# Optimization experiments

Measured on AMD Instinct MI355X. Metric: run time of the kernel, lower is better.

## Reference

```python
import jax, jax.numpy as jnp
import numpy as np

NW, NT, ND = 100000, 10000, 50000
D = 128
E = {"ww": 200000, "wt": 100000, "wd": 150000, "td": 100000, "tt": 50000}


def setup_inputs() -> dict:
    key = jax.random.key(0)
    ks = iter(jax.random.split(key, 40))
    inp = {
        "h_word": jax.random.normal(next(ks), (NW, D), dtype=jnp.float32),
        "h_topic": jax.random.normal(next(ks), (NT, D), dtype=jnp.float32),
        "h_doc": jax.random.normal(next(ks), (ND, D), dtype=jnp.float32),
    }
    for et in ["ww", "wt", "wd", "td", "tt"]:
        inp[f"W_{et}"] = jax.random.normal(next(ks), (D, D), dtype=jnp.float32) * 0.05
        inp[f"b_{et}"] = jax.random.normal(next(ks), (D,), dtype=jnp.float32) * 0.05
    sizes = {"ww": (NW, NW), "wt": (NW, NT), "wd": (NW, ND), "td": (NT, ND), "tt": (NT, NT)}
    for et, (ns, nd) in sizes.items():
        inp[f"src_{et}"] = jax.random.randint(next(ks), (E[et],), 0, ns, dtype=jnp.int32)
        inp[f"dst_{et}"] = jax.random.randint(next(ks), (E[et],), 0, nd, dtype=jnp.int32)
        inp[f"ew_{et}"] = jax.random.uniform(next(ks), (E[et],), dtype=jnp.float32)
    return inp


def _linear(x, W, b):
    # torch nn.Linear: y = x @ W.T + b, W is [out, in]
    return x @ W.T + b


def _mean_agg(h_src, src, dst, ew, n_dst):
    # message m_e = h_src[src_e] * ew_e (u_mul_e), then per-dst mean (fn.mean)
    m = h_src[src] * ew[:, None]                               # [E, D]
    s = jax.ops.segment_sum(m, dst, num_segments=n_dst)        # [n_dst, D]
    cnt = jax.ops.segment_sum(jnp.ones_like(ew), dst, num_segments=n_dst)
    return s / jnp.maximum(cnt, 1.0)[:, None]


def reference(h_word, h_topic, h_doc,
              W_ww, b_ww, W_wt, b_wt, W_wd, b_wd, W_td, b_td, W_tt, b_tt,
              src_ww, dst_ww, ew_ww, src_wt, dst_wt, ew_wt,
              src_wd, dst_wd, ew_wd, src_td, dst_td, ew_td,
              src_tt, dst_tt, ew_tt):
    # DGL loop overwrites src node 'h' in-place -> linears COMPOSE per src type,
    # and messages (resolved at multi_update_all) use the final composed 'h'.
    hw = _linear(_linear(_linear(h_word, W_ww, b_ww), W_wt, b_wt), W_wd, b_wd)
    ht = _linear(_linear(h_topic, W_td, b_td), W_tt, b_tt)
    nw, nt, nd = h_word.shape[0], h_topic.shape[0], h_doc.shape[0]
    # cross-relation 'sum' of per-relation means
    out_word = _mean_agg(hw, src_ww, dst_ww, ew_ww, nw)
    out_topic = _mean_agg(hw, src_wt, dst_wt, ew_wt, nt) + _mean_agg(ht, src_tt, dst_tt, ew_tt, nt)
    out_doc = _mean_agg(hw, src_wd, dst_wd, ew_wd, nd) + _mean_agg(ht, src_td, dst_td, ew_td, nd)
    # relu + dropout (eval mode -> identity); concatenate node types for a single output
    return jnp.concatenate([
        jax.nn.relu(out_word), jax.nn.relu(out_topic), jax.nn.relu(out_doc)
    ], axis=0)
```

## Files before the change

kernel.cpp:

```cpp
#include <hip/hip_runtime.h>
#include <hip/hip_bf16.h>

#define DIM 128
#define NWORD 100000
#define NTOPIC 10000
#define NDOC 50000
#define NOUT (NWORD + NTOPIC + NDOC)

#define E_WW 200000
#define E_WT 100000
#define E_WD 150000
#define E_TD 100000
#define E_TT 50000
#define E_TOT 600000

#define B_WW 0
#define B_WT 100000
#define B_TT 110000
#define B_WD 120000
#define B_TD 170000
#define NSLOT 220000
#define NBLK_SCAN 215

typedef __attribute__((ext_vector_type(8))) short bf16x8;
typedef __attribute__((ext_vector_type(8))) unsigned short u16x8;
typedef __attribute__((ext_vector_type(4))) float f32x4;

__device__ __forceinline__ unsigned short f2bf(float f) {
    __hip_bfloat16 h = __float2bfloat16(f);
    return __builtin_bit_cast(unsigned short, h);
}
__device__ __forceinline__ float b2f(unsigned short u) {
    return __builtin_bit_cast(float, (unsigned)u << 16);
}

__global__ void compose1(const float* __restrict__ W_ww, const float* __restrict__ b_ww,
                         const float* __restrict__ W_wt, const float* __restrict__ b_wt,
                         const float* __restrict__ W_wd, const float* __restrict__ b_wd,
                         const float* __restrict__ W_td, const float* __restrict__ b_td,
                         const float* __restrict__ W_tt, const float* __restrict__ b_tt,
                         float* __restrict__ A, unsigned short* __restrict__ Wbf_t,
                         float* __restrict__ tmpb, float* __restrict__ c_t)
{
    int b = blockIdx.x, j = threadIdx.x;
    if (b < 128) {
        float s = 0.f;
        for (int m = 0; m < 128; ++m) s = fmaf(W_wd[b * 128 + m], W_wt[m * 128 + j], s);
        A[b * 128 + j] = s;
    } else if (b < 256) {
        int k = b - 128;
        float s = 0.f;
        for (int m = 0; m < 128; ++m) s = fmaf(W_tt[j * 128 + m], W_td[m * 128 + k], s);
        Wbf_t[j * 128 + k] = f2bf(s);
    } else if (b == 256) {
        float s = b_wt[j];
        for (int m = 0; m < 128; ++m) s = fmaf(W_wt[j * 128 + m], b_ww[m], s);
        tmpb[j] = s;
    } else {
        float s = b_tt[j];
        for (int m = 0; m < 128; ++m) s = fmaf(W_tt[j * 128 + m], b_td[m], s);
        c_t[j] = s;
    }
}

__global__ void compose2(const float* __restrict__ W_ww, const float* __restrict__ W_wd,
                         const float* __restrict__ b_wd, const float* __restrict__ A,
                         const float* __restrict__ tmpb,
                         unsigned short* __restrict__ Wbf_w, float* __restrict__ c_w)
{
    int b = blockIdx.x, j = threadIdx.x;
    if (b < 128) {
        int k = b;
        float s = 0.f;
        for (int m = 0; m < 128; ++m) s = fmaf(A[j * 128 + m], W_ww[m * 128 + k], s);
        Wbf_w[j * 128 + k] = f2bf(s);
    } else {
        float s = b_wd[j];
        for (int m = 0; m < 128; ++m) s = fmaf(W_wd[j * 128 + m], tmpb[m], s);
        c_w[j] = s;
    }
}

__global__ __launch_bounds__(256) void transform_mfma(
    const float* __restrict__ x, const unsigned short* __restrict__ Wbf,
    const float* __restrict__ bias, unsigned short* __restrict__ y, int ntiles)
{
    __shared__ __attribute__((aligned(16))) unsigned short xs_all[4][16 * 128];
    const int tid = threadIdx.x;
    const int wid = tid >> 6, l = tid & 63;
    char* xs = (char*)xs_all[wid];
    const int l15 = l & 15, l4 = l >> 4;

    bf16x8 wf[8][4];
#pragma unroll
    for (int cg = 0; cg < 8; ++cg)
#pragma unroll
        for (int ki = 0; ki < 4; ++ki)
            wf[cg][ki] = *(const bf16x8*)&Wbf[(cg * 16 + l15) * 128 + ki * 32 + l4 * 8];

    float bj[8];
#pragma unroll
    for (int cg = 0; cg < 8; ++cg) bj[cg] = bias[cg * 16 + l15];

    const int row_s = l >> 2, ch = l & 3;

    for (int tile = blockIdx.x * 4 + wid; tile < ntiles; tile += gridDim.x * 4) {
        const size_t rb = (size_t)tile * 16;

        const float* xr = &x[(rb + row_s) * 128 + ch * 32];
#pragma unroll
        for (int c = 0; c < 4; ++c) {
            float4 u = *(const float4*)(xr + c * 8);
            float4 v = *(const float4*)(xr + c * 8 + 4);
            u16x8 p;
            p[0] = f2bf(u.x); p[1] = f2bf(u.y); p[2] = f2bf(u.z); p[3] = f2bf(u.w);
            p[4] = f2bf(v.x); p[5] = f2bf(v.y); p[6] = f2bf(v.z); p[7] = f2bf(v.w);
            int off = row_s * 256 + ((ch * 64 + c * 16) ^ ((row_s & 7) << 4));
            *(u16x8*)(xs + off) = p;
        }

        f32x4 acc[8];
        const f32x4 zero = {0.f, 0.f, 0.f, 0.f};
#pragma unroll
        for (int cg = 0; cg < 8; ++cg) acc[cg] = zero;

#pragma unroll
        for (int ki = 0; ki < 4; ++ki) {
            int aoff = l15 * 256 + ((ki * 64 + l4 * 16) ^ ((l15 & 7) << 4));
            bf16x8 af = *(const bf16x8*)(xs + aoff);
#pragma unroll
            for (int cg = 0; cg < 8; ++cg)
                acc[cg] = __builtin_amdgcn_mfma_f32_16x16x32_bf16(af, wf[cg][ki], acc[cg], 0, 0, 0);
        }

        unsigned short* yr = &y[(rb + l4 * 4) * 128 + l15];
#pragma unroll
        for (int cg = 0; cg < 8; ++cg)
#pragma unroll
            for (int r = 0; r < 4; ++r)
                yr[r * 128 + cg * 16] = f2bf(acc[cg][r] + bj[cg]);
    }
}

__global__ void hist(const int* __restrict__ dst_ww, const int* __restrict__ dst_wt,
                     const int* __restrict__ dst_wd, const int* __restrict__ dst_td,
                     const int* __restrict__ dst_tt, unsigned* __restrict__ cnt)
{
    int g = blockIdx.x * 256 + threadIdx.x;
    if (g < E_WW)                        atomicAdd(&cnt[B_WW + dst_ww[g]], 1u);
    else if (g < E_WW + E_WT)            atomicAdd(&cnt[B_WT + dst_wt[g - E_WW]], 1u);
    else if (g < E_WW + E_WT + E_WD)     atomicAdd(&cnt[B_WD + dst_wd[g - E_WW - E_WT]], 1u);
    else if (g < E_WW + E_WT + E_WD + E_TD)
        atomicAdd(&cnt[B_TD + dst_td[g - E_WW - E_WT - E_WD]], 1u);
    else if (g < E_TOT)
        atomicAdd(&cnt[B_TT + dst_tt[g - E_WW - E_WT - E_WD - E_TD]], 1u);
}

__global__ __launch_bounds__(256) void scanA(const unsigned* __restrict__ cnt,
                                             unsigned* __restrict__ bsum)
{
    __shared__ unsigned sh[256];
    int t = threadIdx.x;
    int base = blockIdx.x * 1024 + t * 4;
    unsigned s = 0;
#pragma unroll
    for (int i = 0; i < 4; ++i) { int idx = base + i; if (idx < NSLOT) s += cnt[idx]; }
    sh[t] = s; __syncthreads();
    for (int o = 128; o > 0; o >>= 1) { if (t < o) sh[t] += sh[t + o]; __syncthreads(); }
    if (t == 0) bsum[blockIdx.x] = sh[0];
}

__global__ __launch_bounds__(256) void scanB(const unsigned* __restrict__ bsum,
                                             unsigned* __restrict__ boff)
{
    __shared__ unsigned sh[256];
    int t = threadIdx.x;
    unsigned v = (t < NBLK_SCAN) ? bsum[t] : 0u;
    sh[t] = v; __syncthreads();
    for (int o = 1; o < 256; o <<= 1) {
        unsigned x = (t >= o) ? sh[t - o] : 0u;
        __syncthreads();
        sh[t] += x;
        __syncthreads();
    }
    if (t < NBLK_SCAN) boff[t] = sh[t] - v;
}

__global__ __launch_bounds__(256) void scanC(const unsigned* __restrict__ cnt,
                                             const unsigned* __restrict__ boff,
                                             unsigned* __restrict__ offs,
                                             unsigned* __restrict__ curs)
{
    __shared__ unsigned sh[256];
    int t = threadIdx.x;
    int base = blockIdx.x * 1024 + t * 4;
    unsigned c[4]; unsigned s = 0;
#pragma unroll
    for (int i = 0; i < 4; ++i) {
        int idx = base + i;
        c[i] = (idx < NSLOT) ? cnt[idx] : 0u;
        s += c[i];
    }
    sh[t] = s; __syncthreads();
    for (int o = 1; o < 256; o <<= 1) {
        unsigned x = (t >= o) ? sh[t - o] : 0u;
        __syncthreads();
        sh[t] += x;
        __syncthreads();
    }
    unsigned run = boff[blockIdx.x] + sh[t] - s;
#pragma unroll
    for (int i = 0; i < 4; ++i) {
        int idx = base + i;
        if (idx < NSLOT) { offs[idx] = run; curs[idx] = run; run += c[i]; }
    }
}

__global__ void scatter(const int* __restrict__ dst_ww, const int* __restrict__ dst_wt,
                        const int* __restrict__ dst_wd, const int* __restrict__ dst_td,
                        const int* __restrict__ dst_tt,
                        const int* __restrict__ src_ww, const int* __restrict__ src_wt,
                        const int* __restrict__ src_wd, const int* __restrict__ src_td,
                        const int* __restrict__ src_tt,
                        const float* __restrict__ ew_ww, const float* __restrict__ ew_wt,
                        const float* __restrict__ ew_wd, const float* __restrict__ ew_td,
                        const float* __restrict__ ew_tt,
                        unsigned* __restrict__ curs, uint2* __restrict__ se)
{
    int g = blockIdx.x * 256 + threadIdx.x;
    int slotidx, e; unsigned sv; float wv;
    if (g < E_WW)                            { e = g;                             slotidx = B_WW + dst_ww[e]; sv = src_ww[e]; wv = ew_ww[e]; }
    else if (g < E_WW + E_WT)                { e = g - E_WW;                      slotidx = B_WT + dst_wt[e]; sv = src_wt[e]; wv = ew_wt[e]; }
    else if (g < E_WW + E_WT + E_WD)         { e = g - E_WW - E_WT;               slotidx = B_WD + dst_wd[e]; sv = src_wd[e]; wv = ew_wd[e]; }
    else if (g < E_WW + E_WT + E_WD + E_TD)  { e = g - E_WW - E_WT - E_WD;        slotidx = B_TD + dst_td[e]; sv = src_td[e]; wv = ew_td[e]; }
    else if (g < E_TOT)                      { e = g - E_WW - E_WT - E_WD - E_TD; slotidx = B_TT + dst_tt[e]; sv = src_tt[e]; wv = ew_tt[e]; }
    else return;
    unsigned slot = atomicAdd(&curs[slotidx], 1u);
    se[slot] = make_uint2(sv, __builtin_bit_cast(unsigned, wv));
}

__device__ __forceinline__ float4 seg_mean_bf(int slot,
                                              const unsigned* __restrict__ offs,
                                              const unsigned* __restrict__ cnt,
                                              const uint2* __restrict__ se,
                                              const unsigned short* __restrict__ h, int d4)
{
    unsigned off = offs[slot];
    unsigned deg = cnt[slot];
    float ax = 0.f, ay = 0.f, az = 0.f, aw = 0.f;
    for (unsigned j = 0; j < deg; ++j) {
        uint2 e = se[off + j];
        float w = __builtin_bit_cast(float, e.y);
        ushort4 hv = *(const ushort4*)&h[(size_t)e.x * 128 + d4];
        ax = fmaf(b2f(hv.x), w, ax); ay = fmaf(b2f(hv.y), w, ay);
        az = fmaf(b2f(hv.z), w, az); aw = fmaf(b2f(hv.w), w, aw);
    }
    float inv = 1.0f / (float)(deg > 1u ? deg : 1u);
    return float4{ax * inv, ay * inv, az * inv, aw * inv};
}

__global__ void gather(const unsigned* __restrict__ offs, const unsigned* __restrict__ cnt,
                       const uint2* __restrict__ se,
                       const unsigned short* __restrict__ hw,
                       const unsigned short* __restrict__ ht,
                       float* __restrict__ out)
{
    int g = blockIdx.x * 256 + threadIdx.x;
    int n = g >> 5, d4 = (g & 31) << 2;
    if (n >= NOUT) return;
    float4 r;
    if (n < NWORD) {
        r = seg_mean_bf(B_WW + n, offs, cnt, se, hw, d4);
    } else if (n < NWORD + NTOPIC) {
        int i = n - NWORD;
        float4 a = seg_mean_bf(B_WT + i, offs, cnt, se, hw, d4);
        float4 b = seg_mean_bf(B_TT + i, offs, cnt, se, ht, d4);
        r = float4{a.x + b.x, a.y + b.y, a.z + b.z, a.w + b.w};
    } else {
        int i = n - NWORD - NTOPIC;
        float4 a = seg_mean_bf(B_WD + i, offs, cnt, se, hw, d4);
        float4 b = seg_mean_bf(B_TD + i, offs, cnt, se, ht, d4);
        r = float4{a.x + b.x, a.y + b.y, a.z + b.z, a.w + b.w};
    }
    r.x = fmaxf(r.x, 0.f); r.y = fmaxf(r.y, 0.f);
    r.z = fmaxf(r.z, 0.f); r.w = fmaxf(r.w, 0.f);
    *reinterpret_cast<float4*>(&out[(size_t)n * 128 + d4]) = r;
}

extern "C" void kernel_launch(void* const* d_in, const int* in_sizes, int n_in,
                              void* d_out, int out_size, void* d_ws, size_t ws_size,
                              hipStream_t stream) {
    const float* h_word  = (const float*)d_in[0];
    const float* h_topic = (const float*)d_in[1];
    const float* W_ww = (const float*)d_in[3];  const float* b_ww = (const float*)d_in[4];
    const float* W_wt = (const float*)d_in[5];  const float* b_wt = (const float*)d_in[6];
    const float* W_wd = (const float*)d_in[7];  const float* b_wd = (const float*)d_in[8];
    const float* W_td = (const float*)d_in[9];  const float* b_td = (const float*)d_in[10];
    const float* W_tt = (const float*)d_in[11]; const float* b_tt = (const float*)d_in[12];
    const int*   src_ww = (const int*)d_in[13]; const int* dst_ww = (const int*)d_in[14];
    const float* ew_ww  = (const float*)d_in[15];
    const int*   src_wt = (const int*)d_in[16]; const int* dst_wt = (const int*)d_in[17];
    const float* ew_wt  = (const float*)d_in[18];
    const int*   src_wd = (const int*)d_in[19]; const int* dst_wd = (const int*)d_in[20];
    const float* ew_wd  = (const float*)d_in[21];
    const int*   src_td = (const int*)d_in[22]; const int* dst_td = (const int*)d_in[23];
    const float* ew_td  = (const float*)d_in[24];
    const int*   src_tt = (const int*)d_in[25]; const int* dst_tt = (const int*)d_in[26];
    const float* ew_tt  = (const float*)d_in[27];

    float* out = (float*)d_out;

    unsigned short* hw_bf = (unsigned short*)d_ws;
    unsigned short* ht_bf = hw_bf + (size_t)NWORD * 128;
    unsigned short* Wbf_w = ht_bf + (size_t)NTOPIC * 128;
    unsigned short* Wbf_t = Wbf_w + 16384;
    float* fbase = (float*)(Wbf_t + 16384);
    float* c_w   = fbase;
    float* c_t   = c_w + 128;
    float* Amat  = c_t + 128;
    float* tmpb  = Amat + 16384;
    uint2* se    = (uint2*)(tmpb + 128);
    unsigned* cnt  = (unsigned*)(se + E_TOT);
    unsigned* offs = cnt + NSLOT;
    unsigned* curs = offs + NSLOT;
    unsigned* bsum = curs + NSLOT;
    unsigned* boff = bsum + 256;

    hipMemsetAsync(cnt, 0, NSLOT * sizeof(unsigned), stream);

    compose1<<<258, 128, 0, stream>>>(W_ww, b_ww, W_wt, b_wt, W_wd, b_wd, W_td, b_td,
                                      W_tt, b_tt, Amat, Wbf_t, tmpb, c_t);
    compose2<<<129, 128, 0, stream>>>(W_ww, W_wd, b_wd, Amat, tmpb, Wbf_w, c_w);

    hist<<<(E_TOT + 255) / 256, 256, 0, stream>>>(dst_ww, dst_wt, dst_wd, dst_td, dst_tt, cnt);
    scanA<<<NBLK_SCAN, 256, 0, stream>>>(cnt, bsum);
    scanB<<<1, 256, 0, stream>>>(bsum, boff);
    scanC<<<NBLK_SCAN, 256, 0, stream>>>(cnt, boff, offs, curs);
    scatter<<<(E_TOT + 255) / 256, 256, 0, stream>>>(
        dst_ww, dst_wt, dst_wd, dst_td, dst_tt,
        src_ww, src_wt, src_wd, src_td, src_tt,
        ew_ww, ew_wt, ew_wd, ew_td, ew_tt, curs, se);

    transform_mfma<<<512, 256, 0, stream>>>(h_word,  Wbf_w, c_w, hw_bf, NWORD / 16);
    transform_mfma<<<80,  256, 0, stream>>>(h_topic, Wbf_t, c_t, ht_bf, NTOPIC / 16);

    gather<<<(NOUT * 32 + 255) / 256, 256, 0, stream>>>(offs, cnt, se, hw_bf, ht_bf, out);
}
```

Measured before the change: 342.9 us.

## Record per-edge rank in histogram pass and unroll gather loop by four

The histogram kernel now stores the atomic return value as each edge's rank, so the scatter pass writes to offs+rank without a second round of atomics and the cursor array is gone. Degree is now computed from adjacent offsets (an extra sentinel entry) instead of a separate count read. The gather loop is unrolled by four, with four independent row loads in flight; out-of-range lanes are masked by a zero weight and source index 0. This costs an extra rank array write and read of 600k entries, plus some over-reads past segment ends, which are covered by padding se by four entries.

```diff
diff --git a/kernel.cpp b/kernel.cpp
--- a/kernel.cpp
+++ b/kernel.cpp
@@ -142,18 +142,20 @@
     }
 }
 
-__global__ void hist(const int* __restrict__ dst_ww, const int* __restrict__ dst_wt,
-                     const int* __restrict__ dst_wd, const int* __restrict__ dst_td,
-                     const int* __restrict__ dst_tt, unsigned* __restrict__ cnt)
+__global__ void rank_count(const int* __restrict__ dst_ww, const int* __restrict__ dst_wt,
+                           const int* __restrict__ dst_wd, const int* __restrict__ dst_td,
+                           const int* __restrict__ dst_tt,
+                           unsigned* __restrict__ cnt, unsigned* __restrict__ rank)
 {
     int g = blockIdx.x * 256 + threadIdx.x;
-    if (g < E_WW)                        atomicAdd(&cnt[B_WW + dst_ww[g]], 1u);
-    else if (g < E_WW + E_WT)            atomicAdd(&cnt[B_WT + dst_wt[g - E_WW]], 1u);
-    else if (g < E_WW + E_WT + E_WD)     atomicAdd(&cnt[B_WD + dst_wd[g - E_WW - E_WT]], 1u);
-    else if (g < E_WW + E_WT + E_WD + E_TD)
-        atomicAdd(&cnt[B_TD + dst_td[g - E_WW - E_WT - E_WD]], 1u);
-    else if (g < E_TOT)
-        atomicAdd(&cnt[B_TT + dst_tt[g - E_WW - E_WT - E_WD - E_TD]], 1u);
+    int slotidx;
+    if (g < E_WW)                            slotidx = B_WW + dst_ww[g];
+    else if (g < E_WW + E_WT)                slotidx = B_WT + dst_wt[g - E_WW];
+    else if (g < E_WW + E_WT + E_WD)         slotidx = B_WD + dst_wd[g - E_WW - E_WT];
+    else if (g < E_WW + E_WT + E_WD + E_TD)  slotidx = B_TD + dst_td[g - E_WW - E_WT - E_WD];
+    else if (g < E_TOT)                      slotidx = B_TT + dst_tt[g - E_WW - E_WT - E_WD - E_TD];
+    else return;
+    rank[g] = atomicAdd(&cnt[slotidx], 1u);
 }
 
 __global__ __launch_bounds__(256) void scanA(const unsigned* __restrict__ cnt,
@@ -188,8 +190,7 @@
 
 __global__ __launch_bounds__(256) void scanC(const unsigned* __restrict__ cnt,
                                              const unsigned* __restrict__ boff,
-                                             unsigned* __restrict__ offs,
-                                             unsigned* __restrict__ curs)
+                                             unsigned* __restrict__ offs)
 {
     __shared__ unsigned sh[256];
     int t = threadIdx.x;
@@ -212,20 +213,25 @@
 #pragma unroll
     for (int i = 0; i < 4; ++i) {
         int idx = base + i;
-        if (idx < NSLOT) { offs[idx] = run; curs[idx] = run; run += c[i]; }
-    }
-}
-
-__global__ void scatter(const int* __restrict__ dst_ww, const int* __restrict__ dst_wt,
-                        const int* __restrict__ dst_wd, const int* __restrict__ dst_td,
-                        const int* __restrict__ dst_tt,
-                        const int* __restrict__ src_ww, const int* __restrict__ src_wt,
-                        const int* __restrict__ src_wd, const int* __restrict__ src_td,
-                        const int* __restrict__ src_tt,
-                        const float* __restrict__ ew_ww, const float* __restrict__ ew_wt,
-                        const float* __restrict__ ew_wd, const float* __restrict__ ew_td,
-                        const float* __restrict__ ew_tt,
-                        unsigned* __restrict__ curs, uint2* __restrict__ se)
+        if (idx < NSLOT) {
+            offs[idx] = run;
+            run += c[i];
+            if (idx == NSLOT - 1) offs[NSLOT] = run;
+        }
+    }
+}
+
+__global__ void place(const int* __restrict__ dst_ww, const int* __restrict__ dst_wt,
+                      const int* __restrict__ dst_wd, const int* __restrict__ dst_td,
+                      const int* __restrict__ dst_tt,
+                      const int* __restrict__ src_ww, const int* __restrict__ src_wt,
+                      const int* __restrict__ src_wd, const int* __restrict__ src_td,
+                      const int* __restrict__ src_tt,
+                      const float* __restrict__ ew_ww, const float* __restrict__ ew_wt,
+                      const float* __restrict__ ew_wd, const float* __restrict__ ew_td,
+                      const float* __restrict__ ew_tt,
+                      const unsigned* __restrict__ offs, const unsigned* __restrict__ rank,
+                      uint2* __restrict__ se)
 {
     int g = blockIdx.x * 256 + threadIdx.x;
     int slotidx, e; unsigned sv; float wv;
@@ -235,31 +241,48 @@
     else if (g < E_WW + E_WT + E_WD + E_TD)  { e = g - E_WW - E_WT - E_WD;        slotidx = B_TD + dst_td[e]; sv = src_td[e]; wv = ew_td[e]; }
     else if (g < E_TOT)                      { e = g - E_WW - E_WT - E_WD - E_TD; slotidx = B_TT + dst_tt[e]; sv = src_tt[e]; wv = ew_tt[e]; }
     else return;
-    unsigned slot = atomicAdd(&curs[slotidx], 1u);
-    se[slot] = make_uint2(sv, __builtin_bit_cast(unsigned, wv));
+    se[offs[slotidx] + rank[g]] = make_uint2(sv, __builtin_bit_cast(unsigned, wv));
 }
 
 __device__ __forceinline__ float4 seg_mean_bf(int slot,
                                               const unsigned* __restrict__ offs,
-                                              const unsigned* __restrict__ cnt,
                                               const uint2* __restrict__ se,
                                               const unsigned short* __restrict__ h, int d4)
 {
     unsigned off = offs[slot];
-    unsigned deg = cnt[slot];
+    unsigned deg = offs[slot + 1] - off;
     float ax = 0.f, ay = 0.f, az = 0.f, aw = 0.f;
-    for (unsigned j = 0; j < deg; ++j) {
-        uint2 e = se[off + j];
-        float w = __builtin_bit_cast(float, e.y);
-        ushort4 hv = *(const ushort4*)&h[(size_t)e.x * 128 + d4];
-        ax = fmaf(b2f(hv.x), w, ax); ay = fmaf(b2f(hv.y), w, ay);
-        az = fmaf(b2f(hv.z), w, az); aw = fmaf(b2f(hv.w), w, aw);
+    for (unsigned j = 0; j < deg; j += 4) {
+        uint2 r0 = se[off + j];
+        uint2 r1 = se[off + j + 1];
+        uint2 r2 = se[off + j + 2];
+        uint2 r3 = se[off + j + 3];
+        unsigned s0 = r0.x;
+        float    w0 = __builtin_bit_cast(float, r0.y);
+        unsigned s1 = (j + 1 < deg) ? r1.x : 0u;
+        float    w1 = (j + 1 < deg) ? __builtin_bit_cast(float, r1.y) : 0.f;
+        unsigned s2 = (j + 2 < deg) ? r2.x : 0u;
+        float    w2 = (j + 2 < deg) ? __builtin_bit_cast(float, r2.y) : 0.f;
+        unsigned s3 = (j + 3 < deg) ? r3.x : 0u;
+        float    w3 = (j + 3 < deg) ? __builtin_bit_cast(float, r3.y) : 0.f;
+        ushort4 a0 = *(const ushort4*)&h[(size_t)s0 * 128 + d4];
+        ushort4 a1 = *(const ushort4*)&h[(size_t)s1 * 128 + d4];
+        ushort4 a2 = *(const ushort4*)&h[(size_t)s2 * 128 + d4];
+        ushort4 a3 = *(const ushort4*)&h[(size_t)s3 * 128 + d4];
+        ax = fmaf(b2f(a0.x), w0, ax); ay = fmaf(b2f(a0.y), w0, ay);
+        az = fmaf(b2f(a0.z), w0, az); aw = fmaf(b2f(a0.w), w0, aw);
+        ax = fmaf(b2f(a1.x), w1, ax); ay = fmaf(b2f(a1.y), w1, ay);
+        az = fmaf(b2f(a1.z), w1, az); aw = fmaf(b2f(a1.w), w1, aw);
+        ax = fmaf(b2f(a2.x), w2, ax); ay = fmaf(b2f(a2.y), w2, ay);
+        az = fmaf(b2f(a2.z), w2, az); aw = fmaf(b2f(a2.w), w2, aw);
+        ax = fmaf(b2f(a3.x), w3, ax); ay = fmaf(b2f(a3.y), w3, ay);
+        az = fmaf(b2f(a3.z), w3, az); aw = fmaf(b2f(a3.w), w3, aw);
     }
     float inv = 1.0f / (float)(deg > 1u ? deg : 1u);
     return float4{ax * inv, ay * inv, az * inv, aw * inv};
 }
 
-__global__ void gather(const unsigned* __restrict__ offs, const unsigned* __restrict__ cnt,
+__global__ void gather(const unsigned* __restrict__ offs,
                        const uint2* __restrict__ se,
                        const unsigned short* __restrict__ hw,
                        const unsigned short* __restrict__ ht,
@@ -270,16 +293,16 @@
     if (n >= NOUT) return;
     float4 r;
     if (n < NWORD) {
-        r = seg_mean_bf(B_WW + n, offs, cnt, se, hw, d4);
+        r = seg_mean_bf(B_WW + n, offs, se, hw, d4);
     } else if (n < NWORD + NTOPIC) {
         int i = n - NWORD;
-        float4 a = seg_mean_bf(B_WT + i, offs, cnt, se, hw, d4);
-        float4 b = seg_mean_bf(B_TT + i, offs, cnt, se, ht, d4);
+        float4 a = seg_mean_bf(B_WT + i, offs, se, hw, d4);
+        float4 b = seg_mean_bf(B_TT + i, offs, se, ht, d4);
         r = float4{a.x + b.x, a.y + b.y, a.z + b.z, a.w + b.w};
     } else {
         int i = n - NWORD - NTOPIC;
-        float4 a = seg_mean_bf(B_WD + i, offs, cnt, se, hw, d4);
-        float4 b = seg_mean_bf(B_TD + i, offs, cnt, se, ht, d4);
+        float4 a = seg_mean_bf(B_WD + i, offs, se, hw, d4);
+        float4 b = seg_mean_bf(B_TD + i, offs, se, ht, d4);
         r = float4{a.x + b.x, a.y + b.y, a.z + b.z, a.w + b.w};
     }
     r.x = fmaxf(r.x, 0.f); r.y = fmaxf(r.y, 0.f);
@@ -320,10 +343,10 @@
     float* Amat  = c_t + 128;
     float* tmpb  = Amat + 16384;
     uint2* se    = (uint2*)(tmpb + 128);
-    unsigned* cnt  = (unsigned*)(se + E_TOT);
+    unsigned* cnt  = (unsigned*)(se + E_TOT + 4);
     unsigned* offs = cnt + NSLOT;
-    unsigned* curs = offs + NSLOT;
-    unsigned* bsum = curs + NSLOT;
+    unsigned* rank = offs + NSLOT + 1;
+    unsigned* bsum = rank + E_TOT;
     unsigned* boff = bsum + 256;
 
     hipMemsetAsync(cnt, 0, NSLOT * sizeof(unsigned), stream);
@@ -332,17 +355,18 @@
                                       W_tt, b_tt, Amat, Wbf_t, tmpb, c_t);
     compose2<<<129, 128, 0, stream>>>(W_ww, W_wd, b_wd, Amat, tmpb, Wbf_w, c_w);
 
-    hist<<<(E_TOT + 255) / 256, 256, 0, stream>>>(dst_ww, dst_wt, dst_wd, dst_td, dst_tt, cnt);
+    rank_count<<<(E_TOT + 255) / 256, 256, 0, stream>>>(dst_ww, dst_wt, dst_wd, dst_td, dst_tt,
+                                                        cnt, rank);
     scanA<<<NBLK_SCAN, 256, 0, stream>>>(cnt, bsum);
     scanB<<<1, 256, 0, stream>>>(bsum, boff);
-    scanC<<<NBLK_SCAN, 256, 0, stream>>>(cnt, boff, offs, curs);
-    scatter<<<(E_TOT + 255) / 256, 256, 0, stream>>>(
+    scanC<<<NBLK_SCAN, 256, 0, stream>>>(cnt, boff, offs);
+    place<<<(E_TOT + 255) / 256, 256, 0, stream>>>(
         dst_ww, dst_wt, dst_wd, dst_td, dst_tt,
         src_ww, src_wt, src_wd, src_td, src_tt,
-        ew_ww, ew_wt, ew_wd, ew_td, ew_tt, curs, se);
+        ew_ww, ew_wt, ew_wd, ew_td, ew_tt, offs, rank, se);
 
     transform_mfma<<<512, 256, 0, stream>>>(h_word,  Wbf_w, c_w, hw_bf, NWORD / 16);
     transform_mfma<<<80,  256, 0, stream>>>(h_topic, Wbf_t, c_t, ht_bf, NTOPIC / 16);
 
-    gather<<<(NOUT * 32 + 255) / 256, 256, 0, stream>>>(offs, cnt, se, hw_bf, ht_bf, out);
-}
+    gather<<<(NOUT * 32 + 255) / 256, 256, 0, stream>>>(offs, se, hw_bf, ht_bf, out);
+}
```

Result: faster. 312.2 us (-9.0%).
